# Performance work log

Hardware: AMD Instinct MI355X
Metric: run time of the kernel (lower is better)

The kernel has to match this reference:

```python
import jax, jax.numpy as jnp
import numpy as np

N_NODES = 100000
N_EDGES = 1600000
N_FEAT = 128
HIDDEN = 64
N_CLASSES = 16


def setup_inputs() -> dict:
    key = jax.random.key(0)
    ks = jax.random.split(key, 8)
    x = jax.random.normal(ks[0], (N_NODES, N_FEAT), dtype=jnp.float32)
    edge_index = jax.random.randint(ks[1], (2, N_EDGES), 0, N_NODES, dtype=jnp.int64)
    def glorot(k, shape):
        lim = float(np.sqrt(6.0 / (shape[0] + shape[1])))
        return jax.random.uniform(k, shape, jnp.float32, -lim, lim)
    return {
        "x": x,
        "edge_index": edge_index,
        "W0": glorot(ks[2], (N_FEAT, HIDDEN)), "b0": jnp.zeros((HIDDEN,), jnp.float32),
        "W1": glorot(ks[3], (HIDDEN, HIDDEN)), "b1": jnp.zeros((HIDDEN,), jnp.float32),
        "W2": glorot(ks[4], (HIDDEN, 2)),      "b2": jnp.zeros((2,), jnp.float32),
        "Wc": glorot(ks[5], (2, N_CLASSES)),   "bc": jnp.zeros((N_CLASSES,), jnp.float32),
    }


def _gcn_conv(x, W, b, src, dst, norm, n_nodes):
    # GCNConv: D^{-1/2} (A + I) D^{-1/2} X W + b, edges already include self-loops
    h = x @ W                                  # transform first (small dim)
    msg = h[src] * norm[:, None]               # gather + per-edge scale
    agg = jax.ops.segment_sum(msg, dst, num_segments=n_nodes)  # scatter-add
    return agg + b


def reference(x, edge_index, W0, b0, W1, b1, W2, b2, Wc, bc):
    n = x.shape[0]
    loops = jnp.arange(n, dtype=edge_index.dtype)
    src = jnp.concatenate([edge_index[0], loops])
    dst = jnp.concatenate([edge_index[1], loops])
    # degree on destination (col), including self-loops
    deg = jax.ops.segment_sum(jnp.ones_like(dst, dtype=x.dtype), dst, num_segments=n)
    dis = jnp.where(deg > 0, jax.lax.rsqrt(deg), 0.0)
    norm = dis[src] * dis[dst]

    h = _gcn_conv(x, W0, b0, src, dst, norm, n)              # layer 0, no activation
    h = jnp.tanh(_gcn_conv(h, W1, b1, src, dst, norm, n))    # layer 1
    h = jnp.tanh(_gcn_conv(h, W2, b2, src, dst, norm, n))    # layer 2 -> [N, 2]
    embeddings = h
    out = embeddings @ Wc + bc                               # [N, num_classes]
    return (out, embeddings)
```

## Files before the change

### kernel.cpp

```cpp
#include <hip/hip_runtime.h>


#define NF 128
#define NH 64
#define NPB 256
#define MAXNB 512
#define CAP 6144
#define A1G 1024

__global__ void k_init0(const int* __restrict__ ei, int* __restrict__ fmt,
                        int* __restrict__ ccnt, int nb16) {
    int i = blockIdx.x * 256 + threadIdx.x;
    if (i < nb16) ccnt[i] = 0;
    if (i == 0) {
        int f = 1;
        #pragma unroll
        for (int k = 1; k < 32; k += 2) if (ei[k] != 0) f = 0;
        *fmt = f;
    }
}

__global__ void __launch_bounds__(256) k_coarse(
        const int* __restrict__ ei, const int* __restrict__ fmt,
        int* __restrict__ ccnt, int* __restrict__ blockbase, int E, int NB) {
    __shared__ int h[MAXNB];
    int sh = *fmt;
    for (int i = threadIdx.x; i < NB; i += 256) h[i] = 0;
    __syncthreads();
    for (long long e = (long long)blockIdx.x * 256 + threadIdx.x; e < E;
         e += (long long)A1G * 256) {
        int d = ei[(long long)(E + e) << sh];
        atomicAdd(&h[d >> 8], 1);
    }
    __syncthreads();
    for (int b = threadIdx.x; b < NB; b += 256) {
        int c = h[b];
        int base = (c > 0) ? atomicAdd(&ccnt[b * 16], c) : 0;
        blockbase[(long long)blockIdx.x * NB + b] = base;
    }
}

__global__ void __launch_bounds__(512) k_cscan(
        const int* __restrict__ ccnt, int* __restrict__ cstart, int NB) {
    __shared__ int s[512];
    int t = threadIdx.x;
    int c = (t < NB) ? ccnt[t * 16] : 0;
    s[t] = c;
    __syncthreads();
    for (int off = 1; off < 512; off <<= 1) {
        int v = s[t];
        int u = (t >= off) ? s[t - off] : 0;
        __syncthreads();
        s[t] = v + u;
        __syncthreads();
    }
    if (t < NB) cstart[t] = s[t] - c;
}

__global__ void __launch_bounds__(256) k_cscatter(
        const int* __restrict__ ei, const int* __restrict__ fmt,
        const int* __restrict__ cstart, const int* __restrict__ blockbase,
        int* __restrict__ pairs, int E, int NB) {
    __shared__ int h[MAXNB];
    __shared__ int bb[MAXNB];
    int sh = *fmt;
    for (int i = threadIdx.x; i < NB; i += 256) {
        h[i] = 0;
        bb[i] = cstart[i] + blockbase[(long long)blockIdx.x * NB + i];
    }
    __syncthreads();
    for (long long e = (long long)blockIdx.x * 256 + threadIdx.x; e < E;
         e += (long long)A1G * 256) {
        int s = ei[(long long)e << sh];
        int d = ei[(long long)(E + e) << sh];
        int b = d >> 8;
        int r = atomicAdd(&h[b], 1);
        pairs[bb[b] + r] = s | ((d & 255) << 17);
    }
}

__global__ void __launch_bounds__(256) k_bucket(
        const int* __restrict__ pairs, const int* __restrict__ ccnt,
        const int* __restrict__ cstart, int* __restrict__ esrc,
        int* __restrict__ cnt, int* __restrict__ start, float* __restrict__ dis,
        int N) {
    __shared__ int words[CAP];
    __shared__ unsigned char rk[CAP];
    __shared__ int h[NPB];
    __shared__ int hs[NPB];
    int b = blockIdx.x;
    int cs = cstart[b];
    int ec = ccnt[b * 16];
    if (ec > CAP) ec = CAP;
    int t = threadIdx.x;
    for (int i = t; i < ec; i += 256) words[i] = pairs[cs + i];
    h[t] = 0;
    __syncthreads();
    for (int i = t; i < ec; i += 256) {
        int ld = words[i] >> 17;
        rk[i] = (unsigned char)atomicAdd(&h[ld], 1);
    }
    __syncthreads();
    int c = h[t];
    hs[t] = c;
    __syncthreads();
    for (int off = 1; off < 256; off <<= 1) {
        int v = hs[t];
        int u = (t >= off) ? hs[t - off] : 0;
        __syncthreads();
        hs[t] = v + u;
        __syncthreads();
    }
    int node = b * NPB + t;
    if (node < N) {
        cnt[node] = c;
        start[node] = cs + hs[t] - c;
        dis[node] = rsqrtf(1.0f + (float)c);
    }
    for (int i = t; i < ec; i += 256) {
        int w = words[i];
        int ld = w >> 17;
        esrc[cs + (hs[ld] - h[ld]) + rk[i]] = w & 0x1FFFF;
    }
}

#define KP3 68
__global__ void __launch_bounds__(256) k_gemm128(
        const float* __restrict__ X, const float* __restrict__ W,
        const float* __restrict__ dis, short* __restrict__ T16,
        float* __restrict__ rs, int n) {
    __shared__ float xs[64 * KP3];
    __shared__ float Ws[64 * NH];
    __shared__ int rmax[64];
    if (threadIdx.x < 64) rmax[threadIdx.x] = 0;
    long long rowbase = (long long)blockIdx.x * 64;
    int c0 = (threadIdx.x & 15) * 4;
    int r0 = (threadIdx.x >> 4) * 4;
    float4 a0{0,0,0,0}, a1{0,0,0,0}, a2{0,0,0,0}, a3{0,0,0,0};
    #pragma unroll
    for (int ph = 0; ph < 2; ++ph) {
        if (ph) __syncthreads();
        const float4* Wp4 = (const float4*)(W + (long long)ph * 64 * NH);
        for (int i = threadIdx.x; i < 64 * NH / 4; i += 256)
            ((float4*)Ws)[i] = Wp4[i];
        const float* Xp = X + rowbase * NF + ph * 64;
        for (int i = threadIdx.x; i < 1024; i += 256) {
            int r = i >> 4, kk = (i & 15) << 2;
            float4 v = (rowbase + r < n)
                           ? *(const float4*)(Xp + r * NF + kk)
                           : make_float4(0.f, 0.f, 0.f, 0.f);
            *(float4*)&xs[r * KP3 + kk] = v;
        }
        __syncthreads();
        const float* x0 = &xs[(r0 + 0) * KP3];
        const float* x1 = &xs[(r0 + 1) * KP3];
        const float* x2 = &xs[(r0 + 2) * KP3];
        const float* x3 = &xs[(r0 + 3) * KP3];
        const float* Wp0 = &Ws[c0];
        #pragma unroll 4
        for (int k4 = 0; k4 < 16; ++k4) {
            float4 xv0 = *(const float4*)(x0 + k4 * 4);
            float4 xv1 = *(const float4*)(x1 + k4 * 4);
            float4 xv2 = *(const float4*)(x2 + k4 * 4);
            float4 xv3 = *(const float4*)(x3 + k4 * 4);
            float4 wa = *(const float4*)(Wp0 + (k4 * 4 + 0) * NH);
            float4 wb = *(const float4*)(Wp0 + (k4 * 4 + 1) * NH);
            float4 wc = *(const float4*)(Wp0 + (k4 * 4 + 2) * NH);
            float4 wd = *(const float4*)(Wp0 + (k4 * 4 + 3) * NH);
            a0.x += xv0.x * wa.x; a0.y += xv0.x * wa.y; a0.z += xv0.x * wa.z; a0.w += xv0.x * wa.w;
            a1.x += xv1.x * wa.x; a1.y += xv1.x * wa.y; a1.z += xv1.x * wa.z; a1.w += xv1.x * wa.w;
            a2.x += xv2.x * wa.x; a2.y += xv2.x * wa.y; a2.z += xv2.x * wa.z; a2.w += xv2.x * wa.w;
            a3.x += xv3.x * wa.x; a3.y += xv3.x * wa.y; a3.z += xv3.x * wa.z; a3.w += xv3.x * wa.w;
            a0.x += xv0.y * wb.x; a0.y += xv0.y * wb.y; a0.z += xv0.y * wb.z; a0.w += xv0.y * wb.w;
            a1.x += xv1.y * wb.x; a1.y += xv1.y * wb.y; a1.z += xv1.y * wb.z; a1.w += xv1.y * wb.w;
            a2.x += xv2.y * wb.x; a2.y += xv2.y * wb.y; a2.z += xv2.y * wb.z; a2.w += xv2.y * wb.w;
            a3.x += xv3.y * wb.x; a3.y += xv3.y * wb.y; a3.z += xv3.y * wb.z; a3.w += xv3.y * wb.w;
            a0.x += xv0.z * wc.x; a0.y += xv0.z * wc.y; a0.z += xv0.z * wc.z; a0.w += xv0.z * wc.w;
            a1.x += xv1.z * wc.x; a1.y += xv1.z * wc.y; a1.z += xv1.z * wc.z; a1.w += xv1.z * wc.w;
            a2.x += xv2.z * wc.x; a2.y += xv2.z * wc.y; a2.z += xv2.z * wc.z; a2.w += xv2.z * wc.w;
            a3.x += xv3.z * wc.x; a3.y += xv3.z * wc.y; a3.z += xv3.z * wc.z; a3.w += xv3.z * wc.w;
            a0.x += xv0.w * wd.x; a0.y += xv0.w * wd.y; a0.z += xv0.w * wd.z; a0.w += xv0.w * wd.w;
            a1.x += xv1.w * wd.x; a1.y += xv1.w * wd.y; a1.z += xv1.w * wd.z; a1.w += xv1.w * wd.w;
            a2.x += xv2.w * wd.x; a2.y += xv2.w * wd.y; a2.z += xv2.w * wd.z; a2.w += xv2.w * wd.w;
            a3.x += xv3.w * wd.x; a3.y += xv3.w * wd.y; a3.z += xv3.w * wd.z; a3.w += xv3.w * wd.w;
        }
    }
    int row = (int)rowbase + r0;
    float d0 = (row + 0 < n) ? dis[row + 0] : 0.0f;
    float d1 = (row + 1 < n) ? dis[row + 1] : 0.0f;
    float d2 = (row + 2 < n) ? dis[row + 2] : 0.0f;
    float d3 = (row + 3 < n) ? dis[row + 3] : 0.0f;
    a0.x *= d0; a0.y *= d0; a0.z *= d0; a0.w *= d0;
    a1.x *= d1; a1.y *= d1; a1.z *= d1; a1.w *= d1;
    a2.x *= d2; a2.y *= d2; a2.z *= d2; a2.w *= d2;
    a3.x *= d3; a3.y *= d3; a3.z *= d3; a3.w *= d3;
    float m0 = fmaxf(fmaxf(fabsf(a0.x), fabsf(a0.y)), fmaxf(fabsf(a0.z), fabsf(a0.w)));
    float m1 = fmaxf(fmaxf(fabsf(a1.x), fabsf(a1.y)), fmaxf(fabsf(a1.z), fabsf(a1.w)));
    float m2 = fmaxf(fmaxf(fabsf(a2.x), fabsf(a2.y)), fmaxf(fabsf(a2.z), fabsf(a2.w)));
    float m3 = fmaxf(fmaxf(fabsf(a3.x), fabsf(a3.y)), fmaxf(fabsf(a3.z), fabsf(a3.w)));
    atomicMax(&rmax[r0 + 0], __float_as_int(m0));
    atomicMax(&rmax[r0 + 1], __float_as_int(m1));
    atomicMax(&rmax[r0 + 2], __float_as_int(m2));
    atomicMax(&rmax[r0 + 3], __float_as_int(m3));
    __syncthreads();
    float M0 = __int_as_float(rmax[r0 + 0]);
    float M1 = __int_as_float(rmax[r0 + 1]);
    float M2 = __int_as_float(rmax[r0 + 2]);
    float M3 = __int_as_float(rmax[r0 + 3]);
    float i0 = 32767.0f / fmaxf(M0, 1e-20f);
    float i1 = 32767.0f / fmaxf(M1, 1e-20f);
    float i2 = 32767.0f / fmaxf(M2, 1e-20f);
    float i3 = 32767.0f / fmaxf(M3, 1e-20f);
    const float ks = 1.0f / 32767.0f;
    if (row + 0 < n) {
        short4 q = { (short)__float2int_rn(a0.x * i0), (short)__float2int_rn(a0.y * i0),
                     (short)__float2int_rn(a0.z * i0), (short)__float2int_rn(a0.w * i0) };
        *(short4*)&T16[(long long)(row + 0) * NH + c0] = q;
        if (c0 == 0) rs[row + 0] = M0 * ks;
    }
    if (row + 1 < n) {
        short4 q = { (short)__float2int_rn(a1.x * i1), (short)__float2int_rn(a1.y * i1),
                     (short)__float2int_rn(a1.z * i1), (short)__float2int_rn(a1.w * i1) };
        *(short4*)&T16[(long long)(row + 1) * NH + c0] = q;
        if (c0 == 0) rs[row + 1] = M1 * ks;
    }
    if (row + 2 < n) {
        short4 q = { (short)__float2int_rn(a2.x * i2), (short)__float2int_rn(a2.y * i2),
                     (short)__float2int_rn(a2.z * i2), (short)__float2int_rn(a2.w * i2) };
        *(short4*)&T16[(long long)(row + 2) * NH + c0] = q;
        if (c0 == 0) rs[row + 2] = M2 * ks;
    }
    if (row + 3 < n) {
        short4 q = { (short)__float2int_rn(a3.x * i3), (short)__float2int_rn(a3.y * i3),
                     (short)__float2int_rn(a3.z * i3), (short)__float2int_rn(a3.w * i3) };
        *(short4*)&T16[(long long)(row + 3) * NH + c0] = q;
        if (c0 == 0) rs[row + 3] = M3 * ks;
    }
}

#define EDGE_A(J) {                                                           \
    int s_ = __builtin_amdgcn_readlane(sA, (J));                              \
    float f_ = __int_as_float(__builtin_amdgcn_readlane(fAb, (J)));           \
    accA = fmaf(f_, (float)(T + s_ * NH)[lane], accA); }
#define EDGE_B(J) {                                                           \
    int s_ = __builtin_amdgcn_readlane(sB, (J));                              \
    float f_ = __int_as_float(__builtin_amdgcn_readlane(fBb, (J)));           \
    accB = fmaf(f_, (float)(T + s_ * NH)[lane], accB); }

#define SEG_GATHER2                                                           \
    int lane = threadIdx.x & 63;                                              \
    int na = blockIdx.x * 8 + (threadIdx.x >> 6) * 2;                         \
    int nb_ = na + 1;                                                         \
    if (na >= n) return;                                                      \
    bool hasB = (nb_ < n);                                                    \
    float dia = dis[na];                                                      \
    float dib = hasB ? dis[nb_] : 0.0f;                                       \
    int ga = cnt[na], sta = start[na];                                        \
    int gb = hasB ? cnt[nb_] : 0;                                             \
    int stb = hasB ? start[nb_] : 0;                                          \
    float accA = rs[na] * (float)T[na * NH + lane];                           \
    float accB = hasB ? rs[nb_] * (float)T[nb_ * NH + lane] : 0.0f;           \
    int gmax = ga > gb ? ga : gb;                                             \
    for (int base = 0; base < gmax; base += 64) {                             \
        int ma = ga - base; ma = ma < 0 ? 0 : (ma > 64 ? 64 : ma);            \
        int mb = gb - base; mb = mb < 0 ? 0 : (mb > 64 ? 64 : mb);            \
        int sA = 0, sB = 0; float fA = 0.0f, fB = 0.0f;                       \
        if (lane < ma) { sA = esrc[sta + base + lane]; fA = rs[sA]; }         \
        if (lane < mb) { sB = esrc[stb + base + lane]; fB = rs[sB]; }         \
        int fAb = __float_as_int(fA), fBb = __float_as_int(fB);               \
        int mmin = ma < mb ? ma : mb;                                         \
        int j = 0;                                                            \
        for (; j + 3 < mmin; j += 4) {                                        \
            EDGE_A(j + 0) EDGE_B(j + 0)                                       \
            EDGE_A(j + 1) EDGE_B(j + 1)                                       \
            EDGE_A(j + 2) EDGE_B(j + 2)                                       \
            EDGE_A(j + 3) EDGE_B(j + 3)                                       \
        }                                                                     \
        int jA = j, jB = j;                                                   \
        for (; jA + 3 < ma; jA += 4) {                                        \
            EDGE_A(jA + 0) EDGE_A(jA + 1) EDGE_A(jA + 2) EDGE_A(jA + 3)       \
        }                                                                     \
        for (; jA < ma; ++jA) EDGE_A(jA)                                      \
        for (; jB + 3 < mb; jB += 4) {                                        \
            EDGE_B(jB + 0) EDGE_B(jB + 1) EDGE_B(jB + 2) EDGE_B(jB + 3)       \
        }                                                                     \
        for (; jB < mb; ++jB) EDGE_B(jB)                                      \
    }

__global__ void __launch_bounds__(256) k_seg0t(
        const short* __restrict__ T, const float* __restrict__ rs,
        const int* __restrict__ esrc, const int* __restrict__ start,
        const int* __restrict__ cnt, const float* __restrict__ dis,
        const float* __restrict__ b0, const float* __restrict__ W1,
        short* __restrict__ To, float* __restrict__ rso, int n) {
    __shared__ float W1s[NH * NH];
    for (int i = threadIdx.x; i < NH * NH / 4; i += 256)
        ((float4*)W1s)[i] = ((const float4*)W1)[i];
    __syncthreads();
    SEG_GATHER2
    float bv = b0[lane];
    float hA = dia * accA + bv;
    float hB = dib * accB + bv;
    float oA0 = 0.0f, oA1 = 0.0f, oB0 = 0.0f, oB1 = 0.0f;
    #pragma unroll
    for (int c = 0; c < 64; c += 2) {
        float wv0 = W1s[(c + 0) * NH + lane];
        float wv1 = W1s[(c + 1) * NH + lane];
        float ha0 = __int_as_float(__builtin_amdgcn_readlane(__float_as_int(hA), c + 0));
        float ha1 = __int_as_float(__builtin_amdgcn_readlane(__float_as_int(hA), c + 1));
        float hb0 = __int_as_float(__builtin_amdgcn_readlane(__float_as_int(hB), c + 0));
        float hb1 = __int_as_float(__builtin_amdgcn_readlane(__float_as_int(hB), c + 1));
        oA0 = fmaf(ha0, wv0, oA0);
        oA1 = fmaf(ha1, wv1, oA1);
        oB0 = fmaf(hb0, wv0, oB0);
        oB1 = fmaf(hb1, wv1, oB1);
    }
    float oA = (oA0 + oA1) * dia;
    float oB = (oB0 + oB1) * dib;
    float mA = fabsf(oA), mB = fabsf(oB);
    #pragma unroll
    for (int msk = 32; msk; msk >>= 1) {
        mA = fmaxf(mA, __shfl_xor(mA, msk, 64));
        mB = fmaxf(mB, __shfl_xor(mB, msk, 64));
    }
    float iA = 32767.0f / fmaxf(mA, 1e-20f);
    float iB = 32767.0f / fmaxf(mB, 1e-20f);
    const float ks = 1.0f / 32767.0f;
    To[(long long)na * NH + lane] = (short)__float2int_rn(oA * iA);
    if (lane == 0) rso[na] = mA * ks;
    if (hasB) {
        To[(long long)nb_ * NH + lane] = (short)__float2int_rn(oB * iB);
        if (lane == 0) rso[nb_] = mB * ks;
    }
}

__global__ void __launch_bounds__(256) k_seg1f(
        const short* __restrict__ T, const float* __restrict__ rs,
        const int* __restrict__ esrc, const int* __restrict__ start,
        const int* __restrict__ cnt, const float* __restrict__ dis,
        const float* __restrict__ b1, const float* __restrict__ W2,
        float2* __restrict__ t2, int n) {
    SEG_GATHER2
    float bv = b1[lane];
    float2 w = ((const float2*)W2)[lane];
    float tA = tanhf(dia * accA + bv);
    float p0 = tA * w.x, p1 = tA * w.y;
    float tB = hasB ? tanhf(dib * accB + bv) : 0.0f;
    float q0 = tB * w.x, q1 = tB * w.y;
    #pragma unroll
    for (int msk = 32; msk; msk >>= 1) {
        p0 += __shfl_xor(p0, msk, 64);
        p1 += __shfl_xor(p1, msk, 64);
        q0 += __shfl_xor(q0, msk, 64);
        q1 += __shfl_xor(q1, msk, 64);
    }
    if (lane == 0) {
        t2[na] = make_float2(dia * p0, dia * p1);
        if (hasB) t2[nb_] = make_float2(dib * q0, dib * q1);
    }
}

__global__ void __launch_bounds__(256) k_seg2f(
        const float2* __restrict__ T2, const int* __restrict__ esrc,
        const int* __restrict__ start, const int* __restrict__ cnt,
        const float* __restrict__ dis, const float* __restrict__ b2,
        const float* __restrict__ Wc, const float* __restrict__ bc,
        float* __restrict__ out, float* __restrict__ emb, int n) {
    int lane = threadIdx.x & 63;
    int sub = lane >> 4;
    int sl = lane & 15;
    int i = blockIdx.x * 16 + (threadIdx.x >> 6) * 4 + sub;
    if (i >= n) return;
    float di = dis[i];
    int g = cnt[i], st = start[i];
    float a0 = 0.0f, a1 = 0.0f;
    for (int j = sl; j < g; j += 16) {
        float2 v = T2[esrc[st + j]];
        a0 += v.x; a1 += v.y;
    }
    if (sl == 0) {
        float2 s = T2[i];
        a0 += s.x; a1 += s.y;
    }
    #pragma unroll
    for (int msk = 8; msk; msk >>= 1) {
        a0 += __shfl_xor(a0, msk, 64);
        a1 += __shfl_xor(a1, msk, 64);
    }
    float e0 = tanhf(a0 * di + b2[0]);
    float e1 = tanhf(a1 * di + b2[1]);
    if (sl == 0) *(float2*)&emb[(long long)i * 2] = make_float2(e0, e1);
    if (sl < 4) {
        int c = sl * 4;
        float4 o;
        o.x = e0 * Wc[c + 0] + e1 * Wc[16 + c + 0] + bc[c + 0];
        o.y = e0 * Wc[c + 1] + e1 * Wc[16 + c + 1] + bc[c + 1];
        o.z = e0 * Wc[c + 2] + e1 * Wc[16 + c + 2] + bc[c + 2];
        o.w = e0 * Wc[c + 3] + e1 * Wc[16 + c + 3] + bc[c + 3];
        *(float4*)&out[(long long)i * 16 + c] = o;
    }
}

extern "C" void kernel_launch(void* const* d_in, const int* in_sizes, int n_in,
                              void* d_out, int out_size, void* d_ws, size_t ws_size,
                              hipStream_t stream) {
    const float* x  = (const float*)d_in[0];
    const int*   ei = (const int*)  d_in[1];
    const float* W0 = (const float*)d_in[2];
    const float* b0 = (const float*)d_in[3];
    const float* W1 = (const float*)d_in[4];
    const float* b1 = (const float*)d_in[5];
    const float* W2 = (const float*)d_in[6];
    const float* b2 = (const float*)d_in[7];
    const float* Wc = (const float*)d_in[8];
    const float* bc = (const float*)d_in[9];

    int N = in_sizes[0] / NF;
    int E = in_sizes[1] / 2;
    int NB = (N + NPB - 1) / NPB;

    float* out = (float*)d_out;
    float* emb = out + (long long)N * 16;

    short*  T16a = (short*)d_ws;
    char*   r2   = (char*)d_ws + (long long)N * NH * 2;
    short*  T16b = (short*)r2;
    float2* t2   = (float2*)(r2 + (long long)N * NH * 2);
    float*  rs_b = (float*)(r2 + (long long)N * NH * 2 + (long long)N * 8);
    float*  dis  = (float*)((char*)d_ws + (long long)N * NH * 2 + (long long)N * NH * 4);
    float*  rs_a = dis + N;
    int*    cnt   = (int*)(rs_a + N);
    int*    start = cnt + N;
    int*    esrc  = start + N;
    int*    fmt   = esrc + E;

    int* pairs     = (int*)d_ws;
    int* blockbase = pairs + E;
    int* ccnt      = blockbase + (long long)A1G * NB;
    int* cstart    = ccnt + NB * 16;

    int nb_g  = (N + 63) / 64;
    int nb_s2 = (N + 7) / 8;
    int nb_2f = (N + 15) / 16;
    int nb_i0 = (NB * 16 + 255) / 256;

    k_init0   <<<nb_i0, 256, 0, stream>>>(ei, fmt, ccnt, NB * 16);
    k_coarse  <<<A1G, 256, 0, stream>>>(ei, fmt, ccnt, blockbase, E, NB);
    k_cscan   <<<1, 512, 0, stream>>>(ccnt, cstart, NB);
    k_cscatter<<<A1G, 256, 0, stream>>>(ei, fmt, cstart, blockbase, pairs, E, NB);
    k_bucket  <<<NB, 256, 0, stream>>>(pairs, ccnt, cstart, esrc, cnt, start, dis, N);

    k_gemm128 <<<nb_g, 256, 0, stream>>>(x, W0, dis, T16a, rs_a, N);

    k_seg0t   <<<nb_s2, 256, 0, stream>>>(T16a, rs_a, esrc, start, cnt, dis, b0,
                                          W1, T16b, rs_b, N);

    k_seg1f   <<<nb_s2, 256, 0, stream>>>(T16b, rs_b, esrc, start, cnt, dis, b1,
                                          W2, t2, N);

    k_seg2f   <<<nb_2f, 256, 0, stream>>>(t2, esrc, start, cnt, dis, b2, Wc, bc,
                                          out, emb, N);
}
```

Baseline: 331.3 us.

## Move layer-0 feature GEMM to MFMA with split-fp16 precision emulation

Replaces the scalar FMA X@W0 kernel with an MFMA 16x16x32 f16 kernel. Each fp32 operand is split into high and low fp16 parts, and three MFMAs per tile recover near-fp32 accuracy. A small prep kernel lays W0 out in fragment order in scratch so the GEMM can bulk-copy it into LDS. The epilogue now reduces the row max for int16 quantization with wave shuffles instead of LDS atomics. This cuts ALU cost of the GEMM but adds conversion work and an extra launch, and the GEMM may already be bound by reading X.

After: 316.8 us. 1.05x faster.

```diff
diff --git a/kernel.cpp b/kernel.cpp
--- a/kernel.cpp
+++ b/kernel.cpp
@@ -7,6 +7,9 @@
 #define MAXNB 512
 #define CAP 6144
 #define A1G 1024
+
+typedef _Float16 half8 __attribute__((ext_vector_type(8)));
+typedef float f32x4 __attribute__((ext_vector_type(4)));
 
 __global__ void k_init0(const int* __restrict__ ei, int* __restrict__ fmt,
                         int* __restrict__ ccnt, int nb16) {
@@ -124,117 +127,132 @@
     }
 }
 
-#define KP3 68
-__global__ void __launch_bounds__(256) k_gemm128(
-        const float* __restrict__ X, const float* __restrict__ W,
+__global__ void k_wprep(const float* __restrict__ W, short* __restrict__ wf) {
+    int b = blockIdx.x;
+    int kc = b >> 2, ct = b & 3;
+    int t = threadIdx.x;
+    int lane = t & 63;
+    int j0 = (t >> 6) * 2;
+    #pragma unroll
+    for (int jj = 0; jj < 2; ++jj) {
+        int j = j0 + jj;
+        int k = kc * 32 + (lane >> 4) * 8 + j;
+        int col = ct * 16 + (lane & 15);
+        float w = W[k * NH + col];
+        _Float16 h = (_Float16)w;
+        _Float16 l = (_Float16)(w - (float)h);
+        int idx = (b * 64 + lane) * 8 + j;
+        wf[idx] = *(short*)&h;
+        wf[idx + 8192] = *(short*)&l;
+    }
+}
+
+#define KPX 68
+__global__ void __launch_bounds__(256) k_gemmM(
+        const float* __restrict__ X, const short* __restrict__ wfrag,
         const float* __restrict__ dis, short* __restrict__ T16,
         float* __restrict__ rs, int n) {
-    __shared__ float xs[64 * KP3];
-    __shared__ float Ws[64 * NH];
-    __shared__ int rmax[64];
-    if (threadIdx.x < 64) rmax[threadIdx.x] = 0;
+    __shared__ __align__(16) short Wf[16384];
+    __shared__ __align__(16) float xs[64 * KPX];
+    int tid = threadIdx.x;
+    {
+        const int4* src = (const int4*)wfrag;
+        int4* dst = (int4*)Wf;
+        #pragma unroll
+        for (int u = 0; u < 8; ++u) dst[tid + u * 256] = src[tid + u * 256];
+    }
     long long rowbase = (long long)blockIdx.x * 64;
-    int c0 = (threadIdx.x & 15) * 4;
-    int r0 = (threadIdx.x >> 4) * 4;
-    float4 a0{0,0,0,0}, a1{0,0,0,0}, a2{0,0,0,0}, a3{0,0,0,0};
+    int lane = tid & 63;
+    int wid = tid >> 6;
+    f32x4 acc0 = {0,0,0,0}, acc1 = {0,0,0,0}, acc2 = {0,0,0,0}, acc3 = {0,0,0,0};
     #pragma unroll
     for (int ph = 0; ph < 2; ++ph) {
-        if (ph) __syncthreads();
-        const float4* Wp4 = (const float4*)(W + (long long)ph * 64 * NH);
-        for (int i = threadIdx.x; i < 64 * NH / 4; i += 256)
-            ((float4*)Ws)[i] = Wp4[i];
+        __syncthreads();
         const float* Xp = X + rowbase * NF + ph * 64;
-        for (int i = threadIdx.x; i < 1024; i += 256) {
+        #pragma unroll
+        for (int u = 0; u < 4; ++u) {
+            int i = tid + u * 256;
             int r = i >> 4, kk = (i & 15) << 2;
             float4 v = (rowbase + r < n)
                            ? *(const float4*)(Xp + r * NF + kk)
                            : make_float4(0.f, 0.f, 0.f, 0.f);
-            *(float4*)&xs[r * KP3 + kk] = v;
+            *(float4*)&xs[r * KPX + kk] = v;
         }
         __syncthreads();
-        const float* x0 = &xs[(r0 + 0) * KP3];
-        const float* x1 = &xs[(r0 + 1) * KP3];
-        const float* x2 = &xs[(r0 + 2) * KP3];
-        const float* x3 = &xs[(r0 + 3) * KP3];
-        const float* Wp0 = &Ws[c0];
-        #pragma unroll 4
-        for (int k4 = 0; k4 < 16; ++k4) {
-            float4 xv0 = *(const float4*)(x0 + k4 * 4);
-            float4 xv1 = *(const float4*)(x1 + k4 * 4);
-            float4 xv2 = *(const float4*)(x2 + k4 * 4);
-            float4 xv3 = *(const float4*)(x3 + k4 * 4);
-            float4 wa = *(const float4*)(Wp0 + (k4 * 4 + 0) * NH);
-            float4 wb = *(const float4*)(Wp0 + (k4 * 4 + 1) * NH);
-            float4 wc = *(const float4*)(Wp0 + (k4 * 4 + 2) * NH);
-            float4 wd = *(const float4*)(Wp0 + (k4 * 4 + 3) * NH);
-            a0.x += xv0.x * wa.x; a0.y += xv0.x * wa.y; a0.z += xv0.x * wa.z; a0.w += xv0.x * wa.w;
-            a1.x += xv1.x * wa.x; a1.y += xv1.x * wa.y; a1.z += xv1.x * wa.z; a1.w += xv1.x * wa.w;
-            a2.x += xv2.x * wa.x; a2.y += xv2.x * wa.y; a2.z += xv2.x * wa.z; a2.w += xv2.x * wa.w;
-            a3.x += xv3.x * wa.x; a3.y += xv3.x * wa.y; a3.z += xv3.x * wa.z; a3.w += xv3.x * wa.w;
-            a0.x += xv0.y * wb.x; a0.y += xv0.y * wb.y; a0.z += xv0.y * wb.z; a0.w += xv0.y * wb.w;
-            a1.x += xv1.y * wb.x; a1.y += xv1.y * wb.y; a1.z += xv1.y * wb.z; a1.w += xv1.y * wb.w;
-            a2.x += xv2.y * wb.x; a2.y += xv2.y * wb.y; a2.z += xv2.y * wb.z; a2.w += xv2.y * wb.w;
-            a3.x += xv3.y * wb.x; a3.y += xv3.y * wb.y; a3.z += xv3.y * wb.z; a3.w += xv3.y * wb.w;
-            a0.x += xv0.z * wc.x; a0.y += xv0.z * wc.y; a0.z += xv0.z * wc.z; a0.w += xv0.z * wc.w;
-            a1.x += xv1.z * wc.x; a1.y += xv1.z * wc.y; a1.z += xv1.z * wc.z; a1.w += xv1.z * wc.w;
-            a2.x += xv2.z * wc.x; a2.y += xv2.z * wc.y; a2.z += xv2.z * wc.z; a2.w += xv2.z * wc.w;
-            a3.x += xv3.z * wc.x; a3.y += xv3.z * wc.y; a3.z += xv3.z * wc.z; a3.w += xv3.z * wc.w;
-            a0.x += xv0.w * wd.x; a0.y += xv0.w * wd.y; a0.z += xv0.w * wd.z; a0.w += xv0.w * wd.w;
-            a1.x += xv1.w * wd.x; a1.y += xv1.w * wd.y; a1.z += xv1.w * wd.z; a1.w += xv1.w * wd.w;
-            a2.x += xv2.w * wd.x; a2.y += xv2.w * wd.y; a2.z += xv2.w * wd.z; a2.w += xv2.w * wd.w;
-            a3.x += xv3.w * wd.x; a3.y += xv3.w * wd.y; a3.z += xv3.w * wd.z; a3.w += xv3.w * wd.w;
+        #pragma unroll
+        for (int kcl = 0; kcl < 2; ++kcl) {
+            const float* xp =
+                &xs[(wid * 16 + (lane & 15)) * KPX + kcl * 32 + (lane >> 4) * 8];
+            float4 xa = *(const float4*)xp;
+            float4 xb = *(const float4*)(xp + 4);
+            float xv[8] = {xa.x, xa.y, xa.z, xa.w, xb.x, xb.y, xb.z, xb.w};
+            half8 ah, al;
+            #pragma unroll
+            for (int e = 0; e < 8; ++e) {
+                _Float16 h = (_Float16)xv[e];
+                ah[e] = h;
+                al[e] = (_Float16)(xv[e] - (float)h);
+            }
+            int kc = ph * 2 + kcl;
+            {
+                const half8 bh = *(const half8*)&Wf[((kc * 4 + 0) * 64 + lane) * 8];
+                const half8 bl = *(const half8*)&Wf[((kc * 4 + 0) * 64 + lane) * 8 + 8192];
+                acc0 = __builtin_amdgcn_mfma_f32_16x16x32_f16(ah, bh, acc0, 0, 0, 0);
+                acc0 = __builtin_amdgcn_mfma_f32_16x16x32_f16(ah, bl, acc0, 0, 0, 0);
+                acc0 = __builtin_amdgcn_mfma_f32_16x16x32_f16(al, bh, acc0, 0, 0, 0);
+            }
+            {
+                const half8 bh = *(const half8*)&Wf[((kc * 4 + 1) * 64 + lane) * 8];
+                const half8 bl = *(const half8*)&Wf[((kc * 4 + 1) * 64 + lane) * 8 + 8192];
+                acc1 = __builtin_amdgcn_mfma_f32_16x16x32_f16(ah, bh, acc1, 0, 0, 0);
+                acc1 = __builtin_amdgcn_mfma_f32_16x16x32_f16(ah, bl, acc1, 0, 0, 0);
+                acc1 = __builtin_amdgcn_mfma_f32_16x16x32_f16(al, bh, acc1, 0, 0, 0);
+            }
+            {
+                const half8 bh = *(const half8*)&Wf[((kc * 4 + 2) * 64 + lane) * 8];
+                const half8 bl = *(const half8*)&Wf[((kc * 4 + 2) * 64 + lane) * 8 + 8192];
+                acc2 = __builtin_amdgcn_mfma_f32_16x16x32_f16(ah, bh, acc2, 0, 0, 0);
+                acc2 = __builtin_amdgcn_mfma_f32_16x16x32_f16(ah, bl, acc2, 0, 0, 0);
+                acc2 = __builtin_amdgcn_mfma_f32_16x16x32_f16(al, bh, acc2, 0, 0, 0);
+            }
+            {
+                const half8 bh = *(const half8*)&Wf[((kc * 4 + 3) * 64 + lane) * 8];
+                const half8 bl = *(const half8*)&Wf[((kc * 4 + 3) * 64 + lane) * 8 + 8192];
+                acc3 = __builtin_amdgcn_mfma_f32_16x16x32_f16(ah, bh, acc3, 0, 0, 0);
+                acc3 = __builtin_amdgcn_mfma_f32_16x16x32_f16(ah, bl, acc3, 0, 0, 0);
+                acc3 = __builtin_amdgcn_mfma_f32_16x16x32_f16(al, bh, acc3, 0, 0, 0);
+            }
         }
     }
-    int row = (int)rowbase + r0;
-    float d0 = (row + 0 < n) ? dis[row + 0] : 0.0f;
-    float d1 = (row + 1 < n) ? dis[row + 1] : 0.0f;
-    float d2 = (row + 2 < n) ? dis[row + 2] : 0.0f;
-    float d3 = (row + 3 < n) ? dis[row + 3] : 0.0f;
-    a0.x *= d0; a0.y *= d0; a0.z *= d0; a0.w *= d0;
-    a1.x *= d1; a1.y *= d1; a1.z *= d1; a1.w *= d1;
-    a2.x *= d2; a2.y *= d2; a2.z *= d2; a2.w *= d2;
-    a3.x *= d3; a3.y *= d3; a3.z *= d3; a3.w *= d3;
-    float m0 = fmaxf(fmaxf(fabsf(a0.x), fabsf(a0.y)), fmaxf(fabsf(a0.z), fabsf(a0.w)));
-    float m1 = fmaxf(fmaxf(fabsf(a1.x), fabsf(a1.y)), fmaxf(fabsf(a1.z), fabsf(a1.w)));
-    float m2 = fmaxf(fmaxf(fabsf(a2.x), fabsf(a2.y)), fmaxf(fabsf(a2.z), fabsf(a2.w)));
-    float m3 = fmaxf(fmaxf(fabsf(a3.x), fabsf(a3.y)), fmaxf(fabsf(a3.z), fabsf(a3.w)));
-    atomicMax(&rmax[r0 + 0], __float_as_int(m0));
-    atomicMax(&rmax[r0 + 1], __float_as_int(m1));
-    atomicMax(&rmax[r0 + 2], __float_as_int(m2));
-    atomicMax(&rmax[r0 + 3], __float_as_int(m3));
-    __syncthreads();
-    float M0 = __int_as_float(rmax[r0 + 0]);
-    float M1 = __int_as_float(rmax[r0 + 1]);
-    float M2 = __int_as_float(rmax[r0 + 2]);
-    float M3 = __int_as_float(rmax[r0 + 3]);
-    float i0 = 32767.0f / fmaxf(M0, 1e-20f);
-    float i1 = 32767.0f / fmaxf(M1, 1e-20f);
-    float i2 = 32767.0f / fmaxf(M2, 1e-20f);
-    float i3 = 32767.0f / fmaxf(M3, 1e-20f);
+    int rb = (int)rowbase + wid * 16 + (lane >> 4) * 4;
+    float dr0 = (rb + 0 < n) ? dis[rb + 0] : 0.0f;
+    float dr1 = (rb + 1 < n) ? dis[rb + 1] : 0.0f;
+    float dr2 = (rb + 2 < n) ? dis[rb + 2] : 0.0f;
+    float dr3 = (rb + 3 < n) ? dis[rb + 3] : 0.0f;
+    float drs[4] = {dr0, dr1, dr2, dr3};
     const float ks = 1.0f / 32767.0f;
-    if (row + 0 < n) {
-        short4 q = { (short)__float2int_rn(a0.x * i0), (short)__float2int_rn(a0.y * i0),
-                     (short)__float2int_rn(a0.z * i0), (short)__float2int_rn(a0.w * i0) };
-        *(short4*)&T16[(long long)(row + 0) * NH + c0] = q;
-        if (c0 == 0) rs[row + 0] = M0 * ks;
-    }
-    if (row + 1 < n) {
-        short4 q = { (short)__float2int_rn(a1.x * i1), (short)__float2int_rn(a1.y * i1),
-                     (short)__float2int_rn(a1.z * i1), (short)__float2int_rn(a1.w * i1) };
-        *(short4*)&T16[(long long)(row + 1) * NH + c0] = q;
-        if (c0 == 0) rs[row + 1] = M1 * ks;
-    }
-    if (row + 2 < n) {
-        short4 q = { (short)__float2int_rn(a2.x * i2), (short)__float2int_rn(a2.y * i2),
-                     (short)__float2int_rn(a2.z * i2), (short)__float2int_rn(a2.w * i2) };
-        *(short4*)&T16[(long long)(row + 2) * NH + c0] = q;
-        if (c0 == 0) rs[row + 2] = M2 * ks;
-    }
-    if (row + 3 < n) {
-        short4 q = { (short)__float2int_rn(a3.x * i3), (short)__float2int_rn(a3.y * i3),
-                     (short)__float2int_rn(a3.z * i3), (short)__float2int_rn(a3.w * i3) };
-        *(short4*)&T16[(long long)(row + 3) * NH + c0] = q;
-        if (c0 == 0) rs[row + 3] = M3 * ks;
+    int cb = lane & 15;
+    #pragma unroll
+    for (int r = 0; r < 4; ++r) {
+        float v0 = acc0[r] * drs[r];
+        float v1 = acc1[r] * drs[r];
+        float v2 = acc2[r] * drs[r];
+        float v3 = acc3[r] * drs[r];
+        float m = fmaxf(fmaxf(fabsf(v0), fabsf(v1)), fmaxf(fabsf(v2), fabsf(v3)));
+        m = fmaxf(m, __shfl_xor(m, 1, 64));
+        m = fmaxf(m, __shfl_xor(m, 2, 64));
+        m = fmaxf(m, __shfl_xor(m, 4, 64));
+        m = fmaxf(m, __shfl_xor(m, 8, 64));
+        float ir = 32767.0f / fmaxf(m, 1e-20f);
+        int rowg = rb + r;
+        if (rowg < n) {
+            long long base = (long long)rowg * NH;
+            T16[base + 0  + cb] = (short)__float2int_rn(v0 * ir);
+            T16[base + 16 + cb] = (short)__float2int_rn(v1 * ir);
+            T16[base + 32 + cb] = (short)__float2int_rn(v2 * ir);
+            T16[base + 48 + cb] = (short)__float2int_rn(v3 * ir);
+            if (cb == 0) rs[rowg] = m * ks;
+        }
     }
 }
 
@@ -425,6 +443,7 @@
     short*  T16a = (short*)d_ws;
     char*   r2   = (char*)d_ws + (long long)N * NH * 2;
     short*  T16b = (short*)r2;
+    short*  wfrag = (short*)r2;
     float2* t2   = (float2*)(r2 + (long long)N * NH * 2);
     float*  rs_b = (float*)(r2 + (long long)N * NH * 2 + (long long)N * 8);
     float*  dis  = (float*)((char*)d_ws + (long long)N * NH * 2 + (long long)N * NH * 4);
@@ -444,13 +463,15 @@
     int nb_2f = (N + 15) / 16;
     int nb_i0 = (NB * 16 + 255) / 256;
 
+    k_wprep   <<<16, 256, 0, stream>>>(W0, wfrag);
+
     k_init0   <<<nb_i0, 256, 0, stream>>>(ei, fmt, ccnt, NB * 16);
     k_coarse  <<<A1G, 256, 0, stream>>>(ei, fmt, ccnt, blockbase, E, NB);
     k_cscan   <<<1, 512, 0, stream>>>(ccnt, cstart, NB);
     k_cscatter<<<A1G, 256, 0, stream>>>(ei, fmt, cstart, blockbase, pairs, E, NB);
     k_bucket  <<<NB, 256, 0, stream>>>(pairs, ccnt, cstart, esrc, cnt, start, dis, N);
 
-    k_gemm128 <<<nb_g, 256, 0, stream>>>(x, W0, dis, T16a, rs_a, N);
+    k_gemmM   <<<nb_g, 256, 0, stream>>>(x, wfrag, dis, T16a, rs_a, N);
 
     k_seg0t   <<<nb_s2, 256, 0, stream>>>(T16a, rs_a, esrc, start, cnt, dis, b0,
                                           W1, T16b, rs_b, N);
```
